# Kernel optimization log

Measured on AMD Instinct MI355X. Metric: run time of the kernel, lower is better.

The kernel has to match this reference:

```python
import jax, jax.numpy as jnp
import numpy as np

SEQ = 16384
IN_CH = 32
OUT_CH = 32
KSIZE = 16
DIL = 2
OFFSET = 0.1
NK = 11  # number of sub-kernels: 16*(2^11 - 1) = 32752 >= 16384
MULT_BASE = 0.5 ** (1.0 / (SEQ / 4))
# exp weight function multipliers (only first NK entries are used, indexed by l)
MULT = (MULT_BASE ** np.arange(NK)) * (1.0 - OFFSET) + OFFSET


def _interp_linear(k, scale):
    """F.interpolate(mode='linear', align_corners=False) along last axis."""
    L = k.shape[-1]
    Lo = L * scale
    coords = (jnp.arange(Lo, dtype=jnp.float32) + 0.5) / scale - 0.5
    coords = jnp.clip(coords, 0.0, L - 1)
    i0 = jnp.floor(coords).astype(jnp.int32)
    i1 = jnp.minimum(i0 + 1, L - 1)
    w = (coords - i0.astype(jnp.float32)).astype(k.dtype)
    return k[..., i0] * (1.0 - w) + k[..., i1] * w


def _build_long_kernel(kernels, center_kernel):
    # kernels: [NK, 2*O, I, KSIZE] -> synthesized long kernel [O, I, 2*SEQ+1]
    parts = [_interp_linear(kernels[l], DIL ** l) * jnp.asarray(MULT[l], kernels.dtype)
             for l in range(NK)]
    k = jnp.concatenate(parts, axis=-1)              # [2*O, I, T], T >= SEQ
    k = k.reshape(2, OUT_CH, IN_CH, k.shape[-1])
    k = jnp.concatenate([jnp.flip(k[0][..., :SEQ], axis=-1),
                         center_kernel,
                         k[1][..., :SEQ]], axis=-1)  # [O, I, 2*SEQ+1]
    # kernel_norm is computed on first forward and detached
    norm = jax.lax.stop_gradient(jnp.linalg.norm(k, axis=-1, keepdims=True))
    return k / norm


def _fft_conv(x, k):
    # cross-correlation via FFT, padding=SEQ, stride=1
    n = SEQ + 2 * SEQ                                 # padded signal length = 3*SEQ
    klen = 2 * SEQ + 1
    x_pad = jnp.pad(x, ((0, 0), (0, 0), (SEQ, SEQ)))
    Xf = jnp.fft.rfft(x_pad, n=n)                     # [B, I, F]
    Kf = jnp.fft.rfft(k, n=n)                         # [O, I, F]
    Yf = jnp.einsum('bif,oif->bof', Xf, jnp.conj(Kf))
    y = jnp.fft.irfft(Yf, n=n)                        # [B, O, n]
    out_len = n - klen + 1                            # == SEQ
    return y[..., :out_len].astype(x.dtype)


def setup_inputs() -> dict:
    key = jax.random.key(0)
    k1, k2, k3 = jax.random.split(key, 3)
    x = jax.random.normal(k1, (8, IN_CH, SEQ), dtype=jnp.float32)
    kernels = jax.random.normal(k2, (NK, 2 * OUT_CH, IN_CH, KSIZE), dtype=jnp.float32)
    center_kernel = jax.random.normal(k3, (OUT_CH, IN_CH, 1), dtype=jnp.float32)
    return {"x": x, "kernels": kernels, "center_kernel": center_kernel}


def reference(x, kernels, center_kernel):
    k = _build_long_kernel(kernels, center_kernel)
    return _fft_conv(x, k)
```

## Files before the change

kernel.cpp:

```cpp
#include <hip/hip_runtime.h>
#include <hip/hip_bf16.h>
#include <stdint.h>

#define SEQ    16384
#define NKL    11
#define NSTEP  467
#define GSTEPS 8
#define NGRP   ((NSTEP + GSTEPS - 1)/GSTEPS)
#define PAD    128
#define SNLO   1152
#define SNHI   17544
#define SROWS  (SNLO + SNHI)

typedef __attribute__((ext_vector_type(8))) short short8;
typedef __attribute__((ext_vector_type(4))) float f32x4;

__host__ __device__ inline int arrUlo(int a){
  if (a == 0) return 0;
  if (a <= 9) return -(2*(1<<a) - 1);
  int lv = (a <= 18) ? (a-9) : (a-18);
  return -((1<<lv) - 1);
}
__host__ __device__ inline int arrRowsP(int a){ return SEQ - arrUlo(a) + 2*PAD; }
__host__ __device__ inline long arrOff(int a){ long o=0; for (int k=0;k<a;k++) o += arrRowsP(k); return o; }
__host__ __device__ inline long totRows(){ return arrOff(28); }

__device__ inline float multf(int l){ return (float)(pow(0.5, (double)l/4096.0)*0.9 + 0.1); }
__device__ inline float Kv(const float* kern, int l, int g, int o, int i, int p){
  return kern[ (((size_t)((l*2 + g)*32 + o))*32 + i)*16 + p ];
}
__device__ inline ushort bfb(float v){
  return __builtin_bit_cast(ushort, __float2bfloat16(v));
}

struct Step { int arr; int c; int l; int g; int kidx; float coeff; };

__device__ inline Step decode(int st){
  Step r;
  if (st == 0){ r = {0, 0, 0, 0, 0, 1.f}; return r; }
  if (st < 17){ int p = st-1;  r = {0, 1+p,  0, 1, p, 1.f}; return r; }
  if (st < 33){ int p = st-17; r = {0, -1-p, 0, 0, p, 1.f}; return r; }
  if (st < 465){
    int t = st-33; int blk = t/24, k = t%24;
    int l = 1 + blk/2; int g = (blk & 1) ? 0 : 1;
    int s = 1<<l, hs = s>>1, off = 16*(s-1);
    float inv2s = 0.5f/(float)s;
    int arrT = l, arrB1 = 9+l, arrM = 18+l, arrH = (l==1) ? 0 : (8+l);
    if (k < 18){
      int p = k-1; int pp = p < 0 ? 0 : (p > 15 ? 15 : p);
      int c = g ? (1+off+p*s-hs) : (-off-p*s-3*hs);
      r = {arrT, c, l, g, pp, inv2s}; return r;
    }
    int kk = k-18;
    if (g){
      int c3 = 1+off-3*hs, c3h = 1+off-hs, c4 = 1+off+16*s+hs, c4h = 1+off+16*s;
      switch(kk){
        case 0: r = {arrM,  c3,  l, g, 0,  -2.f*inv2s}; return r;
        case 1: r = {arrB1, c3,  l, g, 0,  -inv2s}; return r;
        case 2: r = {arrH,  c3h, l, g, 0,  -1.f}; return r;
        case 3: r = {arrB1, c4,  l, g, 15, -(2.f*s-1.f)*inv2s}; return r;
        case 4: r = {arrM,  c4,  l, g, 15, +2.f*inv2s}; return r;
        default:r = {arrH,  c4h, l, g, 15, -1.f}; return r;
      }
    } else {
      int c3 = -off+hs, c3h = -off, c4 = -off-17*s-hs, c4h = -off-16*s-hs;
      switch(kk){
        case 0: r = {arrB1, c3,  l, g, 0,  -(2.f*s-1.f)*inv2s}; return r;
        case 1: r = {arrM,  c3,  l, g, 0,  +2.f*inv2s}; return r;
        case 2: r = {arrH,  c3h, l, g, 0,  -1.f}; return r;
        case 3: r = {arrM,  c4,  l, g, 15, -2.f*inv2s}; return r;
        case 4: r = {arrB1, c4,  l, g, 15, -inv2s}; return r;
        default:r = {arrH,  c4h, l, g, 15, -1.f}; return r;
      }
    }
  }
  if (st == 465){ r = {13, 16369, 10, 1, 0, 1.f}; return r; }
  r = {13, -16384, 10, 0, 0, 1.f}; return r;
}

__global__ __launch_bounds__(256) void norm_k(const float* __restrict__ kern,
                                              const float* __restrict__ cen,
                                              float* __restrict__ invn){
  int o = blockIdx.x >> 5, i = blockIdx.x & 31, tid = threadIdx.x;
  float mlt[NKL];
  for (int l = 0; l < NKL; l++) mlt[l] = multf(l);
  double acc = 0.0;
  for (int pos = tid; pos < 2*SEQ; pos += 256){
    int r = pos & (SEQ-1);
    int lr = (r >> 4) + 1;
    int l  = 31 - __clz(lr);
    int s  = 1 << l;
    int j  = r - 16*(s - 1);
    float c = (j + 0.5f)/(float)s - 0.5f;
    c = fminf(fmaxf(c, 0.f), 15.f);
    int i0 = (int)floorf(c);
    int i1 = (i0+1 < 15) ? i0+1 : 15;
    float w = c - (float)i0;
    int g = pos >> 14;
    float v = Kv(kern,l,g,o,i,i0)*(1.f-w) + Kv(kern,l,g,o,i,i1)*w;
    v *= mlt[l];
    acc += (double)v * v;
  }
  __shared__ double sred[256];
  sred[tid] = acc; __syncthreads();
  for (int ofs = 128; ofs > 0; ofs >>= 1){ if (tid < ofs) sred[tid] += sred[tid+ofs]; __syncthreads(); }
  if (tid == 0){
    float cc = cen[o*32 + i];
    double tot = sred[0] + (double)cc*cc;
    invn[o*32 + i] = (float)(1.0 / sqrt(tot));
  }
}

__global__ __launch_bounds__(256) void wts_k(const float* __restrict__ kern,
                                             const float* __restrict__ cen,
                                             const float* __restrict__ invn,
                                             __hip_bfloat16* __restrict__ wts){
  int st = blockIdx.x;
  Step sp = decode(st);
  float m = multf(sp.l);
  for (int idx = threadIdx.x; idx < 1024; idx += 256){
    int o = idx >> 5, i = idx & 31;
    float in = invn[o*32 + i];
    float w;
    if (st == 0) w = cen[o*32 + i] * in;
    else         w = m * Kv(kern, sp.l, sp.g, o, i, sp.kidx) * in * sp.coeff;
    int sidx = idx ^ (((o >> 1) & 3) << 3);
    wts[(size_t)st*1024 + sidx] = __float2bfloat16(w);
  }
}

__global__ void setup_k(int4* __restrict__ stab){
  int st = blockIdx.x*256 + threadIdx.x;
  if (st >= NSTEP) return;
  Step sp = decode(st);
  int ulo = arrUlo(sp.arr);
  long base = arrOff(sp.arr) + (sp.c - ulo) + PAD;
  int y = ulo - 255 - sp.c;
  stab[st] = make_int4((int)base, y, SEQ - 1 - sp.c, (int)(base + y + 127));
}

__global__ __launch_bounds__(256) void pfs_k(const float* __restrict__ x,
                                             double* __restrict__ tmp,
                                             float* __restrict__ S1o,
                                             float* __restrict__ S2o,
                                             float* __restrict__ R1o, int b0){
  __shared__ double sc1[256], sc2[256], scr[256];
  __shared__ double t1s, t2s, trs;
  int tid = threadIdx.x;
  int blocal = blockIdx.x >> 5, i = blockIdx.x & 31;
  int b = b0 + blocal;
  const float* xp = x + (((size_t)(b*32 + i)) << 14);
  int n0 = tid * 64;
  double lp = 0.0, lsum = 0.0, rsum = 0.0;
  for (int e = 0; e < 64; e++){
    double xv = (double)xp[n0 + e];
    lsum += lp;
    lp += xv;
    rsum += (double)(n0 + e) * xv;
  }
  sc1[tid] = lp; sc2[tid] = lsum; scr[tid] = rsum;
  __syncthreads();
  if (tid == 0){
    double a1 = 0, a2 = 0, ar = 0;
    for (int t = 0; t < 256; t++){
      double l1 = sc1[t], l2 = sc2[t], lr = scr[t];
      sc1[t] = a1; sc2[t] = a2; scr[t] = ar;
      a2 += 64.0*a1 + l2;
      a1 += l1;
      ar += lr;
    }
    t1s = a1; t2s = a2; trs = ar;
  }
  __syncthreads();
  double s1v = sc1[tid], s2v = sc2[tid], r1v = scr[tid];
  double* tp = tmp + ((size_t)((blocal*32 + i)*256 + tid)) * 12;
  for (int e = 0; e < 64; e++){
    if ((e & 15) == 0){
      int q = e >> 4;
      tp[q*3+0] = s1v; tp[q*3+1] = s2v; tp[q*3+2] = r1v;
    }
    double xv = (double)xp[n0 + e];
    s2v += s1v; s1v += xv; r1v += (double)(n0 + e) * xv;
  }
  float* o1 = S1o + (size_t)blocal * SROWS * 32 + i;
  float* o2 = S2o + (size_t)blocal * SROWS * 32 + i;
  float* o3 = R1o + (size_t)blocal * SROWS * 32 + i;
  double T1 = t1s, T2 = t2s, TR = trs;
  for (int r = tid; r < SNLO; r += 256){
    size_t row = (size_t)r * 32;
    o1[row] = 0.f; o2[row] = 0.f; o3[row] = 0.f;
  }
  for (int r = tid; r < SNHI - SEQ; r += 256){
    size_t row = (size_t)(SEQ + r + SNLO) * 32;
    o1[row] = (float)T1;
    o2[row] = (float)(T2 + (double)r * T1);
    o3[row] = (float)TR;
  }
}

__global__ __launch_bounds__(256) void pfe_k(const float* __restrict__ x,
                                             const double* __restrict__ tmp,
                                             float* __restrict__ S1o,
                                             float* __restrict__ S2o,
                                             float* __restrict__ R1o, int b0){
  int gb = blockIdx.x;
  int blocal = gb >> 7, bx = gb & 127;
  int tid = threadIdx.x;
  int i = tid & 31, sj = tid >> 5;
  int sub = bx*8 + sj;
  int b = b0 + blocal;
  const double* tp = tmp + ((size_t)((blocal*32 + i)*1024 + sub)) * 3;
  double s1v = tp[0], s2v = tp[1], r1v = tp[2];
  const float* xp = x + (((size_t)(b*32 + i)) << 14);
  float* o1 = S1o + (size_t)blocal * SROWS * 32 + i;
  float* o2 = S2o + (size_t)blocal * SROWS * 32 + i;
  float* o3 = R1o + (size_t)blocal * SROWS * 32 + i;
  int n0 = sub * 16;
  for (int e = 0; e < 16; e++){
    int n = n0 + e;
    size_t row = (size_t)(n + SNLO) * 32;
    o1[row] = (float)s1v; o2[row] = (float)s2v; o3[row] = (float)r1v;
    double xv = (double)xp[n];
    s2v += s1v; s1v += xv; r1v += (double)n * xv;
  }
}

#define P1T 261
__global__ __launch_bounds__(256,2) void p1_k(const float* __restrict__ x,
                                              __hip_bfloat16* __restrict__ tr, int b0){
  __shared__ float Xb[4096], Ab[4096], Bb[4096], Db[4096];
  int tid = threadIdx.x;
  int bl = blockIdx.x / P1T, bx = blockIdx.x % P1T;
  int b = b0 + bl;
  int S0 = -192 + bx*64;
  long tR = totRows();
  ushort* trb = (ushort*)tr + (size_t)bl * tR * 32;

  {
    int i = tid >> 3, seg = tid & 7;
    const float* xp = x + (((size_t)(b*32 + i)) << 14);
    for (int e = 0; e < 16; e++){
      int ul = seg*16 + e; int u = S0 + ul;
      Xb[ul*32 + i] = (u >= 0 && u < SEQ) ? xp[u] : 0.f;
    }
  }
  __syncthreads();

  auto storeArr = [&](const float* src, int arr){
    int ulo = arrUlo(arr); long ofs = arrOff(arr);
    unsigned rows = (unsigned)(SEQ - ulo + 2*PAD);
    for (int e2 = 0; e2 < 4; e2++){
      int f2 = e2*256 + tid;
      int ul = f2 >> 4, j = (f2 & 15)*2;
      unsigned p = (unsigned)(S0 + ul - (ulo - PAD));
      if (p < rows){
        ushort2 pk;
        pk.x = bfb(src[ul*32 + j]);
        pk.y = bfb(src[ul*32 + j + 1]);
        *(ushort2*)(trb + ((size_t)(ofs + p))*32 + j) = pk;
      }
    }
  };
  auto storeT = [&](const float* nx, int arr){
    int ulo = arrUlo(arr); long ofs = arrOff(arr);
    unsigned rows = (unsigned)(SEQ - ulo + 2*PAD);
    for (int e2 = 0; e2 < 4; e2++){
      int f2 = e2*256 + tid;
      int ul = f2 >> 4, j = (f2 & 15)*2;
      unsigned p = (unsigned)(S0 + ul - (ulo - PAD));
      if (p < rows){
        ushort2 pk;
        pk.x = bfb(nx[ul*32 + j]     + nx[(ul+1)*32 + j]);
        pk.y = bfb(nx[ul*32 + j + 1] + nx[(ul+1)*32 + j + 1]);
        *(ushort2*)(trb + ((size_t)(ofs + p))*32 + j) = pk;
      }
    }
  };

  {
    const float* cur = Xb; float* nxt = Ab;
    #pragma unroll
    for (int l = 1; l <= 5; l++){
      int sp32 = (1 << (l-1)) * 32;
      int LIM = 130 - (2 << l);
      for (int e2 = 0; e2 < 16; e2++){
        int flat = e2*256 + tid;
        if ((flat >> 5) < LIM)
          nxt[flat] = cur[flat] + 2.f*cur[flat + sp32] + cur[flat + 2*sp32];
      }
      __syncthreads();
      storeT(nxt, l);
      cur = nxt; nxt = (l & 1) ? Bb : Ab;
    }
  }
  __syncthreads();
  {
    for (int e2 = 0; e2 < 16; e2++){
      int flat = e2*256 + tid;
      if ((flat >> 5) < 127){
        Ab[flat] = Xb[flat] + Xb[flat + 32];
        Db[flat] = Xb[flat + 32];
      }
    }
    __syncthreads();
    storeArr(Ab, 10); storeArr(Db, 19);
    float* bc = Ab; float* mc = Db; float* bn = Xb; float* mn = Bb;
    #pragma unroll
    for (int l = 2; l <= 5; l++){
      int sp = 1 << (l-1), sp32 = sp*32;
      int LIM = 129 - (1 << l);
      float fs = (float)sp;
      for (int e2 = 0; e2 < 16; e2++){
        int flat = e2*256 + tid;
        if ((flat >> 5) < LIM){
          float bwv = bc[flat + sp32];
          bn[flat] = bc[flat] + bwv;
          mn[flat] = mc[flat] + mc[flat + sp32] + fs*bwv;
        }
      }
      __syncthreads();
      storeArr(bn, 9 + l); storeArr(mn, 18 + l);
      float* t1 = bc; bc = bn; bn = t1;
      float* t2 = mc; mc = mn; mn = t2;
    }
  }
}

#define G2T 1104
__global__ __launch_bounds__(256) void gen2_k(const float* __restrict__ S1p,
                                              const float* __restrict__ S2p,
                                              const float* __restrict__ R1p,
                                              __hip_bfloat16* __restrict__ tr,
                                              int blBase){
  int tid = threadIdx.x;
  int bl = blockIdx.x / G2T, bx = blockIdx.x % G2T;
  int i = tid & 31, ug = tid >> 5;
  long tR = totRows();
  ushort* trb = (ushort*)tr + (size_t)(blBase + bl) * tR * 32;
  const float* s1 = S1p + (size_t)bl * SROWS * 32 + i;
  const float* s2 = S2p + (size_t)bl * SROWS * 32 + i;
  const float* r1 = R1p + (size_t)bl * SROWS * 32 + i;
  for (int e = 0; e < 2; e++){
    int u = -SNLO + bx*16 + e*8 + ug;
    size_t ns = (size_t)(u + SNLO) * 32;
    float s1_0 = s1[ns], s1_1 = s1[ns + 32];
    float s2_0 = s2[ns], s2_1 = s2[ns + 32];
    float r1_0 = r1[ns];
    {
      unsigned p = (unsigned)(u + PAD);
      if (p < (unsigned)(SEQ + 2*PAD))
        trb[((size_t)(arrOff(0) + p))*32 + i] = bfb(s1_1 - s1_0);
    }
    #pragma unroll
    for (int li = 0; li < 4; li++){
      const int l = 6 + li;
      const int s = 1 << l;
      float sa = s2[ns + (size_t)s*32],      sb = s2[ns + (size_t)(s+1)*32];
      float sc2 = s2[ns + (size_t)(2*s)*32], sd = s2[ns + (size_t)(2*s+1)*32];
      float Tv = (sc2 + sd) - 2.f*(sa + sb) + (s2_0 + s2_1);
      float b1v = s1[ns + (size_t)s*32] - s1_0;
      float mv  = (r1[ns + (size_t)s*32] - r1_0) - (float)u * b1v;
      {
        int ulo = -(2*s - 1);
        unsigned p = (unsigned)(u - (ulo - PAD));
        if (p < (unsigned)(SEQ - ulo + 2*PAD))
          trb[((size_t)(arrOff(l) + p))*32 + i] = bfb(Tv);
      }
      {
        int ulo = -(s - 1);
        unsigned p = (unsigned)(u - (ulo - PAD));
        unsigned rows = (unsigned)(SEQ - ulo + 2*PAD);
        if (p < rows){
          trb[((size_t)(arrOff(9 + l) + p))*32 + i]  = bfb(b1v);
          trb[((size_t)(arrOff(18 + l) + p))*32 + i] = bfb(mv);
        }
      }
    }
  }
}

__device__ inline void gload16(const void* g, void* l){
  __builtin_amdgcn_global_load_lds(
      (const __attribute__((address_space(1))) void*)g,
      (__attribute__((address_space(3))) void*)l, 16, 0, 0);
}

__global__ __launch_bounds__(256) void gemm8_k(const short* __restrict__ tr,
                                               const short* __restrict__ wts,
                                               const int4* __restrict__ stab,
                                               float* __restrict__ out,
                                               int b0, long tR){
  __shared__ int4 sstab[NSTEP];
  __shared__ __align__(16) char smem[33792];
  short* Wlds = (short*)smem;
  int tid = threadIdx.x, wid = tid >> 6, lane = tid & 63;
  int N = gridDim.x;
  int wg = (blockIdx.x & 7) * (N >> 3) + (blockIdx.x >> 3);
  int bl = wg >> 6, T0 = (wg & 63) << 8;
  int b = b0 + bl;
  int rowlane = lane & 15, chunk = lane >> 4;
  const short* trb = tr + (size_t)bl * tR * 32;
  const char* wbase = (const char*)wts;
  int rowbase = wid*64 + rowlane;
  int chunkoff = chunk*8;
  int voffA = rowbase*32 + chunkoff;
  int offw = (rowlane*32 + chunk*8) ^ (((rowlane >> 1) & 3) << 3);
  f32x4 acc00={0,0,0,0}, acc01={0,0,0,0}, acc10={0,0,0,0}, acc11={0,0,0,0};
  f32x4 acc20={0,0,0,0}, acc21={0,0,0,0}, acc30={0,0,0,0}, acc31={0,0,0,0};

  for (int k = tid; k < NSTEP; k += 256) sstab[k] = stab[k];

  auto stageW = [&](int g, int buf){
    const char* src = wbase + (size_t)g*16384 + wid*1024 + lane*16;
    char* dst = smem + buf*16384 + wid*1024;
    #pragma unroll
    for (int k = 0; k < 4; k++)
      gload16(src + k*4096, dst + k*4096);
  };

  short8 a0A,a1A,a2A,a3A, a0B,a1B,a2B,a3B;
  int acA = 0, acB = 0;

#define PREFA(s, A0_,A1_,A2_,A3_, AC) { \
    int sc_ = (s) < NSTEP ? (s) : NSTEP-1; \
    int4 EE = sstab[sc_]; \
    int ey_ = __builtin_amdgcn_readfirstlane(EE.y); \
    int ez_ = __builtin_amdgcn_readfirstlane(EE.z); \
    int ew_ = __builtin_amdgcn_readfirstlane(EE.w); \
    AC = ((s) < NSTEP) && (T0 >= ey_) && (T0 <= ez_); \
    int base_ = T0 - ey_ - 127; \
    int rowsM1_ = ez_ - ey_ + 1; \
    const short* gb = trb + (size_t)ew_ * 32; \
    if (base_ >= 0 && base_ + 255 <= rowsM1_){ \
      const short* p_ = gb + (size_t)base_*32 + voffA; \
      A0_ = *(const short8*)(p_); \
      A1_ = *(const short8*)(p_ + 512); \
      A2_ = *(const short8*)(p_ + 1024); \
      A3_ = *(const short8*)(p_ + 1536); \
    } else { \
      int rel = base_ + rowbase; \
      int r0_ = rel;      r0_ = r0_ < 0 ? 0 : (r0_ > rowsM1_ ? rowsM1_ : r0_); \
      int r1_ = rel + 16; r1_ = r1_ < 0 ? 0 : (r1_ > rowsM1_ ? rowsM1_ : r1_); \
      int r2_ = rel + 32; r2_ = r2_ < 0 ? 0 : (r2_ > rowsM1_ ? rowsM1_ : r2_); \
      int r3_ = rel + 48; r3_ = r3_ < 0 ? 0 : (r3_ > rowsM1_ ? rowsM1_ : r3_); \
      A0_ = *(const short8*)(gb + r0_*32 + chunkoff); \
      A1_ = *(const short8*)(gb + r1_*32 + chunkoff); \
      A2_ = *(const short8*)(gb + r2_*32 + chunkoff); \
      A3_ = *(const short8*)(gb + r3_*32 + chunkoff); } }

#define CONS(kk, cb, A0_,A1_,A2_,A3_, AC) if (AC){ \
    const short* wp = Wlds + (cb)*8192 + (kk)*1024 + offw; \
    short8 w0_ = *(const short8*)wp; \
    short8 w1_ = *(const short8*)(wp + 512); \
    acc00 = __builtin_amdgcn_mfma_f32_16x16x32_bf16(A0_, w0_, acc00, 0,0,0); \
    acc01 = __builtin_amdgcn_mfma_f32_16x16x32_bf16(A0_, w1_, acc01, 0,0,0); \
    acc10 = __builtin_amdgcn_mfma_f32_16x16x32_bf16(A1_, w0_, acc10, 0,0,0); \
    acc11 = __builtin_amdgcn_mfma_f32_16x16x32_bf16(A1_, w1_, acc11, 0,0,0); \
    acc20 = __builtin_amdgcn_mfma_f32_16x16x32_bf16(A2_, w0_, acc20, 0,0,0); \
    acc21 = __builtin_amdgcn_mfma_f32_16x16x32_bf16(A2_, w1_, acc21, 0,0,0); \
    acc30 = __builtin_amdgcn_mfma_f32_16x16x32_bf16(A3_, w0_, acc30, 0,0,0); \
    acc31 = __builtin_amdgcn_mfma_f32_16x16x32_bf16(A3_, w1_, acc31, 0,0,0); }

  stageW(0, 0);
  asm volatile("s_waitcnt vmcnt(0)" ::: "memory");
  __syncthreads();

  PREFA(0, a0A,a1A,a2A,a3A, acA)
  PREFA(1, a0B,a1B,a2B,a3B, acB)
  int cbuf = 0;
  for (int g = 0; g < NGRP; ++g){
    if (g + 1 < NGRP) stageW(g + 1, cbuf ^ 1);
    int sb = g*GSTEPS;
    #pragma unroll
    for (int k = 0; k < GSTEPS; k += 2){
      CONS(k,   cbuf, a0A,a1A,a2A,a3A, acA)
      PREFA(sb+k+2, a0A,a1A,a2A,a3A, acA)
      CONS(k+1, cbuf, a0B,a1B,a2B,a3B, acB)
      PREFA(sb+k+3, a0B,a1B,a2B,a3B, acB)
    }
    asm volatile("s_waitcnt vmcnt(8)" ::: "memory");
    __builtin_amdgcn_s_barrier();
    cbuf ^= 1;
  }

  {
    float* Ob = (float*)smem;
    int r0e = wid*64 + chunk*4;
    for (int r = 0; r < 4; r++){
      Ob[(r0e +  0 + r)*33 + rowlane]      = acc00[r];
      Ob[(r0e +  0 + r)*33 + rowlane + 16] = acc01[r];
      Ob[(r0e + 16 + r)*33 + rowlane]      = acc10[r];
      Ob[(r0e + 16 + r)*33 + rowlane + 16] = acc11[r];
      Ob[(r0e + 32 + r)*33 + rowlane]      = acc20[r];
      Ob[(r0e + 32 + r)*33 + rowlane + 16] = acc21[r];
      Ob[(r0e + 48 + r)*33 + rowlane]      = acc30[r];
      Ob[(r0e + 48 + r)*33 + rowlane + 16] = acc31[r];
    }
    __syncthreads();
    for (int r = 0; r < 32; r++){
      int flat = r*256 + tid;
      int o = flat >> 8, t = flat & 255;
      out[((size_t)(b*32 + o) << 14) + T0 + t] = Ob[t*33 + o];
    }
  }
}

extern "C" void kernel_launch(void* const* d_in, const int* in_sizes, int n_in,
                              void* d_out, int out_size, void* d_ws, size_t ws_size,
                              hipStream_t stream) {
  const float* x    = (const float*)d_in[0];
  const float* kern = (const float*)d_in[1];
  const float* cen  = (const float*)d_in[2];
  float* out = (float*)d_out;
  char* ws = (char*)d_ws;

  long tR = totRows();
  size_t oWts  = 4096;
  size_t wtsBytes = (size_t)NGRP * 16384;
  size_t oStab = (oWts + wtsBytes + 255) & ~(size_t)255;
  size_t oTr   = (oStab + (size_t)NSTEP*16 + 1023) & ~(size_t)1023;

  size_t trB_per  = (size_t)tR * 64;
  size_t sB_per   = (size_t)SROWS * 128;
  size_t tmpB_per = (size_t)32*256*12*8;

  int CH = 1, SC = 1;
  {
    int cc[9] = {8,8,8,4,4,4,2,2,1};
    int ss[9] = {4,2,1,4,2,1,2,1,1};
    for (int ci = 0; ci < 9; ci++){
      size_t need = oTr + (size_t)cc[ci]*trB_per + (size_t)ss[ci]*(3*sB_per + tmpB_per);
      if (need <= ws_size){ CH = cc[ci]; SC = ss[ci]; break; }
    }
  }
  size_t oS1  = oTr + (size_t)CH * trB_per;
  size_t oS2  = oS1 + (size_t)SC * sB_per;
  size_t oR1  = oS2 + (size_t)SC * sB_per;
  size_t oTmp = oR1 + (size_t)SC * sB_per;

  float* invn = (float*)ws;
  __hip_bfloat16* wts = (__hip_bfloat16*)(ws + oWts);
  int4* stab = (int4*)(ws + oStab);
  __hip_bfloat16* tr = (__hip_bfloat16*)(ws + oTr);
  float* S1 = (float*)(ws + oS1);
  float* S2 = (float*)(ws + oS2);
  float* R1 = (float*)(ws + oR1);
  double* tmp = (double*)(ws + oTmp);

  norm_k<<<1024, 256, 0, stream>>>(kern, cen, invn);
  wts_k<<<NSTEP, 256, 0, stream>>>(kern, cen, invn, wts);
  setup_k<<<2, 256, 0, stream>>>(stab);

  for (int b0 = 0; b0 < 8; b0 += CH){
    p1_k<<<CH*P1T, 256, 0, stream>>>(x, tr, b0);
    for (int s0 = 0; s0 < CH; s0 += SC){
      pfs_k<<<SC*32, 256, 0, stream>>>(x, tmp, S1, S2, R1, b0 + s0);
      pfe_k<<<SC*128, 256, 0, stream>>>(x, tmp, S1, S2, R1, b0 + s0);
      gen2_k<<<SC*G2T, 256, 0, stream>>>(S1, S2, R1, tr, s0);
    }
    gemm8_k<<<CH*64, 256, 0, stream>>>((const short*)tr, (const short*)wts, stab, out, b0, tR);
  }
}
```

Baseline: 570.9 us.

## Split GEMM reduction across two workgroups per tile with atomic accumulation

The main GEMM kernel now splits the 467-step reduction into two halves at group GSPLIT, so each output tile is handled by two workgroups and the grid doubles. Partial results are combined with atomicAdd into an output that is zeroed with a memset first. The step table is read straight from global memory instead of being staged in LDS, and the readfirstlane scalarization is dropped. The aim is better occupancy and load balance across CUs. The cost is atomic traffic, an extra memset, non-deterministic summation order, and possibly slower per-step table lookups.

Result: slower. 600.4 us (+5.2%).

```diff
diff --git a/kernel.cpp b/kernel.cpp
--- a/kernel.cpp
+++ b/kernel.cpp
@@ -7,6 +7,7 @@
 #define NSTEP  467
 #define GSTEPS 8
 #define NGRP   ((NSTEP + GSTEPS - 1)/GSTEPS)
+#define GSPLIT 30
 #define PAD    128
 #define SNLO   1152
 #define SNHI   17544
@@ -385,19 +386,25 @@
       (__attribute__((address_space(3))) void*)l, 16, 0, 0);
 }
 
-__global__ __launch_bounds__(256) void gemm8_k(const short* __restrict__ tr,
+__global__ __launch_bounds__(256) void gemm9_k(const short* __restrict__ tr,
                                                const short* __restrict__ wts,
                                                const int4* __restrict__ stab,
                                                float* __restrict__ out,
                                                int b0, long tR){
-  __shared__ int4 sstab[NSTEP];
   __shared__ __align__(16) char smem[33792];
   short* Wlds = (short*)smem;
   int tid = threadIdx.x, wid = tid >> 6, lane = tid & 63;
   int N = gridDim.x;
   int wg = (blockIdx.x & 7) * (N >> 3) + (blockIdx.x >> 3);
-  int bl = wg >> 6, T0 = (wg & 63) << 8;
+  int bl = wg >> 7;
+  int tile = (wg >> 1) & 63;
+  int h = wg & 1;
+  int T0 = tile << 8;
   int b = b0 + bl;
+  int gLo = h ? GSPLIT : 0;
+  int gHi = h ? NGRP : GSPLIT;
+  int sLo = gLo * GSTEPS;
+  int sHiS = h ? NSTEP : GSPLIT*GSTEPS;
   int rowlane = lane & 15, chunk = lane >> 4;
   const short* trb = tr + (size_t)bl * tR * 32;
   const char* wbase = (const char*)wts;
@@ -408,8 +415,6 @@
   f32x4 acc00={0,0,0,0}, acc01={0,0,0,0}, acc10={0,0,0,0}, acc11={0,0,0,0};
   f32x4 acc20={0,0,0,0}, acc21={0,0,0,0}, acc30={0,0,0,0}, acc31={0,0,0,0};
 
-  for (int k = tid; k < NSTEP; k += 256) sstab[k] = stab[k];
-
   auto stageW = [&](int g, int buf){
     const char* src = wbase + (size_t)g*16384 + wid*1024 + lane*16;
     char* dst = smem + buf*16384 + wid*1024;
@@ -423,14 +428,11 @@
 
 #define PREFA(s, A0_,A1_,A2_,A3_, AC) { \
     int sc_ = (s) < NSTEP ? (s) : NSTEP-1; \
-    int4 EE = sstab[sc_]; \
-    int ey_ = __builtin_amdgcn_readfirstlane(EE.y); \
-    int ez_ = __builtin_amdgcn_readfirstlane(EE.z); \
-    int ew_ = __builtin_amdgcn_readfirstlane(EE.w); \
-    AC = ((s) < NSTEP) && (T0 >= ey_) && (T0 <= ez_); \
-    int base_ = T0 - ey_ - 127; \
-    int rowsM1_ = ez_ - ey_ + 1; \
-    const short* gb = trb + (size_t)ew_ * 32; \
+    int4 EE = stab[sc_]; \
+    AC = ((s) < sHiS) && (T0 >= EE.y) && (T0 <= EE.z); \
+    int base_ = T0 - EE.y - 127; \
+    int rowsM1_ = EE.z - EE.y + 1; \
+    const short* gb = trb + (size_t)EE.w * 32; \
     if (base_ >= 0 && base_ + 255 <= rowsM1_){ \
       const short* p_ = gb + (size_t)base_*32 + voffA; \
       A0_ = *(const short8*)(p_); \
@@ -461,15 +463,15 @@
     acc30 = __builtin_amdgcn_mfma_f32_16x16x32_bf16(A3_, w0_, acc30, 0,0,0); \
     acc31 = __builtin_amdgcn_mfma_f32_16x16x32_bf16(A3_, w1_, acc31, 0,0,0); }
 
-  stageW(0, 0);
+  stageW(gLo, 0);
   asm volatile("s_waitcnt vmcnt(0)" ::: "memory");
   __syncthreads();
 
-  PREFA(0, a0A,a1A,a2A,a3A, acA)
-  PREFA(1, a0B,a1B,a2B,a3B, acB)
+  PREFA(sLo+0, a0A,a1A,a2A,a3A, acA)
+  PREFA(sLo+1, a0B,a1B,a2B,a3B, acB)
   int cbuf = 0;
-  for (int g = 0; g < NGRP; ++g){
-    if (g + 1 < NGRP) stageW(g + 1, cbuf ^ 1);
+  for (int g = gLo; g < gHi; ++g){
+    if (g + 1 < gHi) stageW(g + 1, cbuf ^ 1);
     int sb = g*GSTEPS;
     #pragma unroll
     for (int k = 0; k < GSTEPS; k += 2){
@@ -500,7 +502,7 @@
     for (int r = 0; r < 32; r++){
       int flat = r*256 + tid;
       int o = flat >> 8, t = flat & 255;
-      out[((size_t)(b*32 + o) << 14) + T0 + t] = Ob[t*33 + o];
+      atomicAdd(&out[((size_t)(b*32 + o) << 14) + T0 + t], Ob[t*33 + o]);
     }
   }
 }
@@ -547,6 +549,7 @@
   float* R1 = (float*)(ws + oR1);
   double* tmp = (double*)(ws + oTmp);
 
+  hipMemsetAsync(d_out, 0, (size_t)out_size * sizeof(float), stream);
   norm_k<<<1024, 256, 0, stream>>>(kern, cen, invn);
   wts_k<<<NSTEP, 256, 0, stream>>>(kern, cen, invn, wts);
   setup_k<<<2, 256, 0, stream>>>(stab);
@@ -558,6 +561,6 @@
       pfe_k<<<SC*128, 256, 0, stream>>>(x, tmp, S1, S2, R1, b0 + s0);
       gen2_k<<<SC*G2T, 256, 0, stream>>>(S1, S2, R1, tr, s0);
     }
-    gemm8_k<<<CH*64, 256, 0, stream>>>((const short*)tr, (const short*)wts, stab, out, b0, tR);
-  }
-}
+    gemm9_k<<<CH*128, 256, 0, stream>>>((const short*)tr, (const short*)wts, stab, out, b0, tR);
+  }
+}
```

## Fuse independent prep kernels into combined launches and double-buffer prefix-sum stage

Applied to the files above, without the earlier changes.

Merges norm, setup, p1 and the prefix-scan start stage into one launch, and wts with the prefix-scan end stage into another, dispatching by block index. When workspace allows, gen2 for one chunk runs in the same launch as pfe for the next chunk using double-buffered S arrays. The prefix-scan start now runs for all batches up front, and the padding fills move into pfe. The aim is fewer launches and idle gaps between them, at the cost of 64KB static LDS on every fused block, which may lower occupancy for the lighter bodies.

After: 467.9 us, median of 2. -18.0%, faster.

```diff
diff --git a/kernel.cpp b/kernel.cpp
--- a/kernel.cpp
+++ b/kernel.cpp
@@ -11,6 +11,8 @@
 #define SNLO   1152
 #define SNHI   17544
 #define SROWS  (SNLO + SNHI)
+#define P1T    261
+#define G2T    1104
 
 typedef __attribute__((ext_vector_type(8))) short short8;
 typedef __attribute__((ext_vector_type(4))) float f32x4;
@@ -78,10 +80,11 @@
   r = {13, -16384, 10, 0, 0, 1.f}; return r;
 }
 
-__global__ __launch_bounds__(256) void norm_k(const float* __restrict__ kern,
-                                              const float* __restrict__ cen,
-                                              float* __restrict__ invn){
-  int o = blockIdx.x >> 5, i = blockIdx.x & 31, tid = threadIdx.x;
+
+__device__ void normBody(const float* __restrict__ kern, const float* __restrict__ cen,
+                         float* __restrict__ invn, int bid, int tid, char* shm){
+  double* sred = (double*)shm;
+  int o = bid >> 5, i = bid & 31;
   float mlt[NKL];
   for (int l = 0; l < NKL; l++) mlt[l] = multf(l);
   double acc = 0.0;
@@ -101,7 +104,6 @@
     v *= mlt[l];
     acc += (double)v * v;
   }
-  __shared__ double sred[256];
   sred[tid] = acc; __syncthreads();
   for (int ofs = 128; ofs > 0; ofs >>= 1){ if (tid < ofs) sred[tid] += sred[tid+ofs]; __syncthreads(); }
   if (tid == 0){
@@ -111,14 +113,22 @@
   }
 }
 
-__global__ __launch_bounds__(256) void wts_k(const float* __restrict__ kern,
-                                             const float* __restrict__ cen,
-                                             const float* __restrict__ invn,
-                                             __hip_bfloat16* __restrict__ wts){
-  int st = blockIdx.x;
+__device__ void setupBody(int4* __restrict__ stab, int bid, int tid){
+  int st = bid*256 + tid;
+  if (st >= NSTEP) return;
+  Step sp = decode(st);
+  int ulo = arrUlo(sp.arr);
+  long base = arrOff(sp.arr) + (sp.c - ulo) + PAD;
+  int y = ulo - 255 - sp.c;
+  stab[st] = make_int4((int)base, y, SEQ - 1 - sp.c, (int)(base + y + 127));
+}
+
+__device__ void wtsBody(const float* __restrict__ kern, const float* __restrict__ cen,
+                        const float* __restrict__ invn, __hip_bfloat16* __restrict__ wts,
+                        int st, int tid){
   Step sp = decode(st);
   float m = multf(sp.l);
-  for (int idx = threadIdx.x; idx < 1024; idx += 256){
+  for (int idx = tid; idx < 1024; idx += 256){
     int o = idx >> 5, i = idx & 31;
     float in = invn[o*32 + i];
     float w;
@@ -129,26 +139,13 @@
   }
 }
 
-__global__ void setup_k(int4* __restrict__ stab){
-  int st = blockIdx.x*256 + threadIdx.x;
-  if (st >= NSTEP) return;
-  Step sp = decode(st);
-  int ulo = arrUlo(sp.arr);
-  long base = arrOff(sp.arr) + (sp.c - ulo) + PAD;
-  int y = ulo - 255 - sp.c;
-  stab[st] = make_int4((int)base, y, SEQ - 1 - sp.c, (int)(base + y + 127));
-}
-
-__global__ __launch_bounds__(256) void pfs_k(const float* __restrict__ x,
-                                             double* __restrict__ tmp,
-                                             float* __restrict__ S1o,
-                                             float* __restrict__ S2o,
-                                             float* __restrict__ R1o, int b0){
-  __shared__ double sc1[256], sc2[256], scr[256];
-  __shared__ double t1s, t2s, trs;
-  int tid = threadIdx.x;
-  int blocal = blockIdx.x >> 5, i = blockIdx.x & 31;
-  int b = b0 + blocal;
+__device__ void pfsBody(const float* __restrict__ x, double* __restrict__ tmp,
+                        double* __restrict__ tmpT, int bid, int tid, char* shm){
+  double* sc1 = (double*)shm;
+  double* sc2 = sc1 + 256;
+  double* scr = sc2 + 256;
+  double* tots = scr + 256;
+  int b = bid >> 5, i = bid & 31;
   const float* xp = x + (((size_t)(b*32 + i)) << 14);
   int n0 = tid * 64;
   double lp = 0.0, lsum = 0.0, rsum = 0.0;
@@ -169,11 +166,11 @@
       a1 += l1;
       ar += lr;
     }
-    t1s = a1; t2s = a2; trs = ar;
+    tots[0] = a1; tots[1] = a2; tots[2] = ar;
   }
   __syncthreads();
   double s1v = sc1[tid], s2v = sc2[tid], r1v = scr[tid];
-  double* tp = tmp + ((size_t)((blocal*32 + i)*256 + tid)) * 12;
+  double* tp = tmp + ((size_t)((b*32 + i)*256 + tid)) * 12;
   for (int e = 0; e < 64; e++){
     if ((e & 15) == 0){
       int q = e >> 4;
@@ -182,39 +179,26 @@
     double xv = (double)xp[n0 + e];
     s2v += s1v; s1v += xv; r1v += (double)(n0 + e) * xv;
   }
-  float* o1 = S1o + (size_t)blocal * SROWS * 32 + i;
-  float* o2 = S2o + (size_t)blocal * SROWS * 32 + i;
-  float* o3 = R1o + (size_t)blocal * SROWS * 32 + i;
-  double T1 = t1s, T2 = t2s, TR = trs;
-  for (int r = tid; r < SNLO; r += 256){
-    size_t row = (size_t)r * 32;
-    o1[row] = 0.f; o2[row] = 0.f; o3[row] = 0.f;
-  }
-  for (int r = tid; r < SNHI - SEQ; r += 256){
-    size_t row = (size_t)(SEQ + r + SNLO) * 32;
-    o1[row] = (float)T1;
-    o2[row] = (float)(T2 + (double)r * T1);
-    o3[row] = (float)TR;
-  }
-}
-
-__global__ __launch_bounds__(256) void pfe_k(const float* __restrict__ x,
-                                             const double* __restrict__ tmp,
-                                             float* __restrict__ S1o,
-                                             float* __restrict__ S2o,
-                                             float* __restrict__ R1o, int b0){
-  int gb = blockIdx.x;
+  if (tid == 0){
+    double* tt = tmpT + (size_t)(b*32 + i)*3;
+    tt[0] = tots[0]; tt[1] = tots[1]; tt[2] = tots[2];
+  }
+}
+
+__device__ void pfeBody(const float* __restrict__ x, const double* __restrict__ tmp,
+                        const double* __restrict__ tmpT,
+                        float* __restrict__ S1c, float* __restrict__ S2c, float* __restrict__ R1c,
+                        int gb, int tid, int b0){
   int blocal = gb >> 7, bx = gb & 127;
-  int tid = threadIdx.x;
   int i = tid & 31, sj = tid >> 5;
   int sub = bx*8 + sj;
   int b = b0 + blocal;
-  const double* tp = tmp + ((size_t)((blocal*32 + i)*1024 + sub)) * 3;
+  const double* tp = tmp + ((size_t)((b*32 + i)*1024 + sub)) * 3;
   double s1v = tp[0], s2v = tp[1], r1v = tp[2];
   const float* xp = x + (((size_t)(b*32 + i)) << 14);
-  float* o1 = S1o + (size_t)blocal * SROWS * 32 + i;
-  float* o2 = S2o + (size_t)blocal * SROWS * 32 + i;
-  float* o3 = R1o + (size_t)blocal * SROWS * 32 + i;
+  float* o1 = S1c + (size_t)blocal * SROWS * 32 + i;
+  float* o2 = S2c + (size_t)blocal * SROWS * 32 + i;
+  float* o3 = R1c + (size_t)blocal * SROWS * 32 + i;
   int n0 = sub * 16;
   for (int e = 0; e < 16; e++){
     int n = n0 + e;
@@ -223,17 +207,33 @@
     double xv = (double)xp[n];
     s2v += s1v; s1v += xv; r1v += (double)n * xv;
   }
-}
-
-#define P1T 261
-__global__ __launch_bounds__(256,2) void p1_k(const float* __restrict__ x,
-                                              __hip_bfloat16* __restrict__ tr, int b0){
-  __shared__ float Xb[4096], Ab[4096], Bb[4096], Db[4096];
-  int tid = threadIdx.x;
-  int bl = blockIdx.x / P1T, bx = blockIdx.x % P1T;
+  float* p1b = S1c + (size_t)blocal * SROWS * 32;
+  float* p2b = S2c + (size_t)blocal * SROWS * 32;
+  float* p3b = R1c + (size_t)blocal * SROWS * 32;
+  int flat = bx*256 + tid;
+  for (int idx = flat; idx < SNLO*32; idx += 32768){
+    p1b[idx] = 0.f; p2b[idx] = 0.f; p3b[idx] = 0.f;
+  }
+  const double* tt = tmpT + (size_t)b*32*3;
+  for (int idx = flat; idx < (SNHI-SEQ)*32; idx += 32768){
+    int r = idx >> 5, ii = idx & 31;
+    double T1 = tt[ii*3], T2 = tt[ii*3+1], TR = tt[ii*3+2];
+    size_t ofs = (size_t)(SEQ + SNLO) * 32 + idx;
+    p1b[ofs] = (float)T1;
+    p2b[ofs] = (float)(T2 + (double)r * T1);
+    p3b[ofs] = (float)TR;
+  }
+}
+
+__device__ void p1Body(const float* __restrict__ x, __hip_bfloat16* __restrict__ tr,
+                       int bid, int tid, char* shm, int b0, long tR){
+  float* Xb = (float*)shm;
+  float* Ab = Xb + 4096;
+  float* Bb = Ab + 4096;
+  float* Db = Bb + 4096;
+  int bl = bid / P1T, bx = bid % P1T;
   int b = b0 + bl;
   int S0 = -192 + bx*64;
-  long tR = totRows();
   ushort* trb = (ushort*)tr + (size_t)bl * tR * 32;
 
   {
@@ -326,17 +326,13 @@
   }
 }
 
-#define G2T 1104
-__global__ __launch_bounds__(256) void gen2_k(const float* __restrict__ S1p,
-                                              const float* __restrict__ S2p,
-                                              const float* __restrict__ R1p,
-                                              __hip_bfloat16* __restrict__ tr,
-                                              int blBase){
-  int tid = threadIdx.x;
-  int bl = blockIdx.x / G2T, bx = blockIdx.x % G2T;
+__device__ void gen2Body(const float* __restrict__ S1p, const float* __restrict__ S2p,
+                         const float* __restrict__ R1p, __hip_bfloat16* __restrict__ tr,
+                         int gb0, int nG, int tid, int s0, long tR){
+  int gb = (gb0 & 7) * (nG >> 3) + (gb0 >> 3);
+  int bl = gb / G2T, bx = gb - bl*G2T;
   int i = tid & 31, ug = tid >> 5;
-  long tR = totRows();
-  ushort* trb = (ushort*)tr + (size_t)(blBase + bl) * tR * 32;
+  ushort* trb = (ushort*)tr + (size_t)(s0 + bl) * tR * 32;
   const float* s1 = S1p + (size_t)bl * SROWS * 32 + i;
   const float* s2 = S2p + (size_t)bl * SROWS * 32 + i;
   const float* r1 = R1p + (size_t)bl * SROWS * 32 + i;
@@ -377,6 +373,60 @@
       }
     }
   }
+}
+
+
+__global__ __launch_bounds__(256) void fuseA_k(const float* __restrict__ x,
+                                               const float* __restrict__ kern,
+                                               const float* __restrict__ cen,
+                                               float* __restrict__ invn,
+                                               int4* __restrict__ stab,
+                                               double* __restrict__ tmp,
+                                               double* __restrict__ tmpT,
+                                               __hip_bfloat16* __restrict__ tr,
+                                               int nP1, int nNorm, int nPfs, int b0, long tR){
+  __shared__ __align__(16) char shm[65536];
+  int bid = blockIdx.x, tid = threadIdx.x;
+  if (bid < nP1){ p1Body(x, tr, bid, tid, shm, b0, tR); return; }
+  bid -= nP1;
+  if (bid < nNorm){ normBody(kern, cen, invn, bid, tid, shm); return; }
+  bid -= nNorm;
+  if (nNorm > 0 && bid < 2){ setupBody(stab, bid, tid); return; }
+  if (nNorm > 0) bid -= 2;
+  if (bid < nPfs) pfsBody(x, tmp, tmpT, bid, tid, shm);
+}
+
+__global__ __launch_bounds__(256) void fuseB_k(const float* __restrict__ kern,
+                                               const float* __restrict__ cen,
+                                               const float* __restrict__ invn,
+                                               __hip_bfloat16* __restrict__ wts,
+                                               const float* __restrict__ x,
+                                               const double* __restrict__ tmp,
+                                               const double* __restrict__ tmpT,
+                                               float* __restrict__ S1c, float* __restrict__ S2c,
+                                               float* __restrict__ R1c,
+                                               int nWts, int nPfe, int b0){
+  int bid = blockIdx.x, tid = threadIdx.x;
+  if (bid < nWts){ wtsBody(kern, cen, invn, wts, bid, tid); return; }
+  bid -= nWts;
+  if (bid < nPfe) pfeBody(x, tmp, tmpT, S1c, S2c, R1c, bid, tid, b0);
+}
+
+__global__ __launch_bounds__(256) void fuseC_k(const float* __restrict__ S1a,
+                                               const float* __restrict__ S2a,
+                                               const float* __restrict__ R1a,
+                                               __hip_bfloat16* __restrict__ tr,
+                                               int nGen2, int s0g, long tR,
+                                               const float* __restrict__ x,
+                                               const double* __restrict__ tmp,
+                                               const double* __restrict__ tmpT,
+                                               float* __restrict__ S1b, float* __restrict__ S2b,
+                                               float* __restrict__ R1b,
+                                               int nPfe, int b0p){
+  int bid = blockIdx.x, tid = threadIdx.x;
+  if (bid < nGen2){ gen2Body(S1a, S2a, R1a, tr, bid, nGen2, tid, s0g, tR); return; }
+  bid -= nGen2;
+  if (bid < nPfe) pfeBody(x, tmp, tmpT, S1b, S2b, R1b, bid, tid, b0p);
 }
 
 __device__ inline void gload16(const void* g, void* l){
@@ -518,46 +568,80 @@
   size_t oWts  = 4096;
   size_t wtsBytes = (size_t)NGRP * 16384;
   size_t oStab = (oWts + wtsBytes + 255) & ~(size_t)255;
-  size_t oTr   = (oStab + (size_t)NSTEP*16 + 1023) & ~(size_t)1023;
-
-  size_t trB_per  = (size_t)tR * 64;
-  size_t sB_per   = (size_t)SROWS * 128;
-  size_t tmpB_per = (size_t)32*256*12*8;
-
-  int CH = 1, SC = 1;
-  {
-    int cc[9] = {8,8,8,4,4,4,2,2,1};
-    int ss[9] = {4,2,1,4,2,1,2,1,1};
-    for (int ci = 0; ci < 9; ci++){
-      size_t need = oTr + (size_t)cc[ci]*trB_per + (size_t)ss[ci]*(3*sB_per + tmpB_per);
-      if (need <= ws_size){ CH = cc[ci]; SC = ss[ci]; break; }
-    }
-  }
-  size_t oS1  = oTr + (size_t)CH * trB_per;
-  size_t oS2  = oS1 + (size_t)SC * sB_per;
-  size_t oR1  = oS2 + (size_t)SC * sB_per;
-  size_t oTmp = oR1 + (size_t)SC * sB_per;
+  size_t oTmp  = (oStab + (size_t)NSTEP*16 + 1023) & ~(size_t)1023;
+  size_t tmpBytes  = (size_t)8*32*256*12*8;
+  size_t tmpTBytes = (size_t)8*32*3*8;
+  size_t oTr   = (oTmp + tmpBytes + tmpTBytes + 1023) & ~(size_t)1023;
+
+  size_t trB_per = (size_t)tR * 64;
+  size_t sB_per  = (size_t)SROWS * 128;
 
   float* invn = (float*)ws;
   __hip_bfloat16* wts = (__hip_bfloat16*)(ws + oWts);
   int4* stab = (int4*)(ws + oStab);
+  double* tmp  = (double*)(ws + oTmp);
+  double* tmpT = (double*)(ws + oTmp + tmpBytes);
   __hip_bfloat16* tr = (__hip_bfloat16*)(ws + oTr);
-  float* S1 = (float*)(ws + oS1);
-  float* S2 = (float*)(ws + oS2);
-  float* R1 = (float*)(ws + oR1);
-  double* tmp = (double*)(ws + oTmp);
-
-  norm_k<<<1024, 256, 0, stream>>>(kern, cen, invn);
-  wts_k<<<NSTEP, 256, 0, stream>>>(kern, cen, invn, wts);
-  setup_k<<<2, 256, 0, stream>>>(stab);
-
-  for (int b0 = 0; b0 < 8; b0 += CH){
-    p1_k<<<CH*P1T, 256, 0, stream>>>(x, tr, b0);
-    for (int s0 = 0; s0 < CH; s0 += SC){
-      pfs_k<<<SC*32, 256, 0, stream>>>(x, tmp, S1, S2, R1, b0 + s0);
-      pfe_k<<<SC*128, 256, 0, stream>>>(x, tmp, S1, S2, R1, b0 + s0);
-      gen2_k<<<SC*G2T, 256, 0, stream>>>(S1, S2, R1, tr, s0);
-    }
-    gemm8_k<<<CH*64, 256, 0, stream>>>((const short*)tr, (const short*)wts, stab, out, b0, tR);
-  }
-}
+
+  int CH = 0, SC = 1, DUP = 1;
+  {
+    int scs[7] = {8,4,4,2,2,1,1};
+    int dps[7] = {1,2,1,2,1,2,1};
+    for (int ci = 0; ci < 7; ci++){
+      size_t need = oTr + 8*trB_per + (size_t)3*dps[ci]*scs[ci]*sB_per;
+      if (need <= ws_size){ CH = 8; SC = scs[ci]; DUP = dps[ci]; break; }
+    }
+    if (CH == 0){
+      int cc[5] = {4,4,2,2,1};
+      int ss[5] = {4,2,2,1,1};
+      for (int ci = 0; ci < 5; ci++){
+        size_t need = oTr + (size_t)cc[ci]*trB_per + (size_t)3*ss[ci]*sB_per;
+        if (need <= ws_size){ CH = cc[ci]; SC = ss[ci]; DUP = 1; break; }
+      }
+      if (CH == 0){ CH = 1; SC = 1; DUP = 1; }
+    }
+  }
+  size_t oS = oTr + (size_t)CH * trB_per;
+  auto S1p = [&](int p){ return (float*)(ws + oS + ((size_t)(0*DUP + p))*SC*sB_per); };
+  auto S2p = [&](int p){ return (float*)(ws + oS + ((size_t)(1*DUP + p))*SC*sB_per); };
+  auto R1p = [&](int p){ return (float*)(ws + oS + ((size_t)(2*DUP + p))*SC*sB_per); };
+
+  if (CH == 8){
+    int nch = 8 / SC;
+    fuseA_k<<<8*P1T + 1024 + 2 + 256, 256, 0, stream>>>(x, kern, cen, invn, stab, tmp, tmpT, tr,
+                                                        8*P1T, 1024, 256, 0, tR);
+    fuseB_k<<<NSTEP + SC*128, 256, 0, stream>>>(kern, cen, invn, wts, x, tmp, tmpT,
+                                                S1p(0), S2p(0), R1p(0), NSTEP, SC*128, 0);
+    for (int k = 0; k < nch; k++){
+      int pa = (DUP == 2) ? (k & 1) : 0;
+      int pb = (DUP == 2) ? ((k + 1) & 1) : 0;
+      bool nxt = (k + 1 < nch);
+      if (DUP == 2 && nxt){
+        fuseC_k<<<SC*G2T + SC*128, 256, 0, stream>>>(S1p(pa), S2p(pa), R1p(pa), tr, SC*G2T, k*SC, tR,
+                                                     x, tmp, tmpT, S1p(pb), S2p(pb), R1p(pb),
+                                                     SC*128, (k+1)*SC);
+      } else {
+        fuseC_k<<<SC*G2T, 256, 0, stream>>>(S1p(pa), S2p(pa), R1p(pa), tr, SC*G2T, k*SC, tR,
+                                            x, tmp, tmpT, S1p(0), S2p(0), R1p(0), 0, 0);
+        if (nxt)
+          fuseB_k<<<SC*128, 256, 0, stream>>>(kern, cen, invn, wts, x, tmp, tmpT,
+                                              S1p(0), S2p(0), R1p(0), 0, SC*128, (k+1)*SC);
+      }
+    }
+    gemm8_k<<<8*64, 256, 0, stream>>>((const short*)tr, (const short*)wts, stab, out, 0, tR);
+  } else {
+    for (int b0 = 0; b0 < 8; b0 += CH){
+      fuseA_k<<<CH*P1T + (b0 == 0 ? 1024 + 2 + 256 : 0), 256, 0, stream>>>(
+          x, kern, cen, invn, stab, tmp, tmpT, tr,
+          CH*P1T, b0 == 0 ? 1024 : 0, b0 == 0 ? 256 : 0, b0, tR);
+      for (int s0 = 0; s0 < CH; s0 += SC){
+        fuseB_k<<<(b0 == 0 && s0 == 0 ? NSTEP : 0) + SC*128, 256, 0, stream>>>(
+            kern, cen, invn, wts, x, tmp, tmpT, S1p(0), S2p(0), R1p(0),
+            (b0 == 0 && s0 == 0) ? NSTEP : 0, SC*128, b0 + s0);
+        fuseC_k<<<SC*G2T, 256, 0, stream>>>(S1p(0), S2p(0), R1p(0), tr, SC*G2T, s0, tR,
+                                            x, tmp, tmpT, S1p(0), S2p(0), R1p(0), 0, 0);
+      }
+      gemm8_k<<<CH*64, 256, 0, stream>>>((const short*)tr, (const short*)wts, stab, out, b0, tR);
+    }
+  }
+}
```
